# Optimization experiments

Measured on AMD Instinct MI355X. Metric: run time of the kernel, lower is better.

Reference implementation:

```python
import jax, jax.numpy as jnp
import numpy as np

N_NODES = 100000
N_EDGES = 1600000
IN = 128
HID = 128
EPS = 1e-5


def setup_inputs() -> dict:
    key = jax.random.key(0)
    ks = jax.random.split(key, 20)
    def lin(k, fi, fo):
        return jax.random.normal(k, (fi, fo), dtype=jnp.float32) / np.sqrt(fi)
    inp = {
        'x': jax.random.normal(ks[0], (N_NODES, IN), dtype=jnp.float32),
        'src': jax.random.randint(ks[1], (N_EDGES,), 0, N_NODES),
        'dst': jax.random.randint(ks[2], (N_EDGES,), 0, N_NODES),
        # SAGEConv layer 1..3: fc_self, fc_neigh, bias
        'Wself1': lin(ks[3], IN, HID), 'Wneigh1': lin(ks[4], IN, HID), 'b1': jnp.zeros((HID,), jnp.float32),
        'Wself2': lin(ks[5], HID, HID), 'Wneigh2': lin(ks[6], HID, HID), 'b2': jnp.zeros((HID,), jnp.float32),
        'Wself3': lin(ks[7], HID, HID), 'Wneigh3': lin(ks[8], HID, HID), 'b3': jnp.zeros((HID,), jnp.float32),
        # shared BatchNorm1d(hid)
        'gamma': jnp.ones((HID,), jnp.float32), 'beta': jnp.zeros((HID,), jnp.float32),
        # decoder MLP hid->hid->hid->1
        'Wd1': lin(ks[9], HID, HID), 'bd1': jnp.zeros((HID,), jnp.float32),
        'Wd2': lin(ks[10], HID, HID), 'bd2': jnp.zeros((HID,), jnp.float32),
        'Wd3': lin(ks[11], HID, 1), 'bd3': jnp.zeros((1,), jnp.float32),
    }
    return inp


def _sage_conv(h, src, dst, deg, Wself, Wneigh, b, n):
    # mean aggregation over in-neighbors: gather + segment-sum + divide
    neigh_sum = jax.ops.segment_sum(h[src], dst, num_segments=n)  # [N, F]
    neigh_mean = neigh_sum / deg[:, None]
    return h @ Wself + neigh_mean @ Wneigh + b


def _batch_norm(h, gamma, beta):
    mu = jnp.mean(h, axis=0)
    var = jnp.mean(jnp.square(h - mu), axis=0)  # biased var, as torch BN training
    return gamma * (h - mu) * jax.lax.rsqrt(var + EPS) + beta


def reference(x, src, dst, Wself1, Wneigh1, b1, Wself2, Wneigh2, b2,
              Wself3, Wneigh3, b3, gamma, beta, Wd1, bd1, Wd2, bd2, Wd3, bd3):
    n = x.shape[0]
    deg = jax.ops.segment_sum(jnp.ones_like(dst, dtype=x.dtype), dst, num_segments=n)
    deg = jnp.maximum(deg, 1.0)
    h = _sage_conv(x, src, dst, deg, Wself1, Wneigh1, b1, n)
    h = jax.nn.relu(_batch_norm(h, gamma, beta))  # dropout = identity (eval)
    h = _sage_conv(h, src, dst, deg, Wself2, Wneigh2, b2, n)
    h = jax.nn.relu(_batch_norm(h, gamma, beta))
    h = _sage_conv(h, src, dst, deg, Wself3, Wneigh3, b3, n)
    # decoder MLP
    h = jax.nn.relu(h @ Wd1 + bd1)
    h = jax.nn.relu(h @ Wd2 + bd2)
    return h @ Wd3 + bd3  # [N, 1]
```

## Files before the change

kernel.cpp:

```cpp
#include <hip/hip_runtime.h>

typedef unsigned short u16;
typedef unsigned int u32;
using bf16x8 = __attribute__((ext_vector_type(8))) __bf16;
using f32x4  = __attribute__((ext_vector_type(4))) float;

#define CAP 48

__global__ void SAGE_79328045957727_kernel() {}

__device__ __forceinline__ float bf2f(u16 u) {
  union { u32 i; float f; } v; v.i = ((u32)u) << 16; return v.f;
}
__device__ __forceinline__ u16 f2bf(float f) {
  union { float f; u32 i; } v; v.f = f;
  u32 x = v.i;
  return (u16)((x + 0x7FFFu + ((x >> 16) & 1u)) >> 16);
}


__global__ void zero_kernel(int* p, int n) {
  int i = blockIdx.x * 256 + threadIdx.x;
  if (i < n) p[i] = 0;
}


__global__ __launch_bounds__(256) void build_kernel(
    const int* __restrict__ src, const int* __restrict__ dst,
    int* __restrict__ deg, int* __restrict__ csr, int E, int npart,
    const float* __restrict__ x, u16* __restrict__ xb, long nelem4,
    const float* w0, const float* w1, const float* w2, const float* w3,
    const float* w4, const float* w5, const float* w6, const float* w7,
    u16* __restrict__ wt) {
  int b = blockIdx.x;
  if (b < 1024) {
    int p = b & 7;
    int brank = b >> 3;
    int lo = p * npart, hi = lo + npart;
    for (int i = brank * 256 + threadIdx.x; i < E; i += 128 * 256) {
      int dv = dst[i];
      if (dv >= lo && dv < hi) {
        int pos = atomicAdd(&deg[dv], 1);
        if (pos < CAP) csr[(size_t)dv * CAP + pos] = src[i];
      }
    }
  } else if (b < 1280) {
    long t = (long)(b - 1024) * 256 + threadIdx.x;
    for (long i4 = t; i4 < nelem4; i4 += 256 * 256) {
      float4 v = ((const float4*)x)[i4];
      u32* op = (u32*)(xb + i4 * 4);
      op[0] = ((u32)f2bf(v.y) << 16) | (u32)f2bf(v.x);
      op[1] = ((u32)f2bf(v.w) << 16) | (u32)f2bf(v.z);
    }
  } else {
    int tg = (b - 1280) * 256 + threadIdx.x;
    for (int k = 0; k < 8; ++k) {
      int idx = tg + k * 16384;
      int m = idx >> 14;
      int i = idx & 16383;
      const float* W = m == 0 ? w0 : m == 1 ? w1 : m == 2 ? w2 : m == 3 ? w3
                     : m == 4 ? w4 : m == 5 ? w5 : m == 6 ? w6 : w7;
      int r = i >> 7, c = i & 127;
      wt[(size_t)m * 16384 + (size_t)c * 128 + r] = f2bf(W[i]);
    }
  }
}


template <int BNIN>
__global__ __launch_bounds__(256) void gather_mean_kernel(
    const u16* __restrict__ H, const int* __restrict__ csr,
    const int* __restrict__ deg, const float* __restrict__ stats,
    const float* __restrict__ gamma, const float* __restrict__ beta,
    u16* __restrict__ M, int N, float invN) {
  __shared__ float sSc[128], sSh[128];
  if (BNIN) {
    int t = threadIdx.x;
    if (t < 128) {
      float mu = stats[t] * invN;
      float var = stats[128 + t] * invN - mu * mu;
      float is = rsqrtf(var + 1e-5f);
      float sc = gamma[t] * is;
      sSc[t] = sc;
      sSh[t] = beta[t] - mu * sc;
    }
    __syncthreads();
  }
  int node = blockIdx.x * 16 + (threadIdx.x >> 4);
  if (node >= N) return;
  int lane = threadIdx.x & 15;
  int fo = lane * 8;
  float sc[8], sh[8];
  if (BNIN) {
    for (int j = 0; j < 8; ++j) { sc[j] = sSc[fo + j]; sh[j] = sSh[fo + j]; }
  }
  const int* nl = csr + (size_t)node * CAP;
  int d = deg[node];
  int dm = d < CAP ? d : CAP;
  float a0=0.f,a1=0.f,a2=0.f,a3=0.f,a4=0.f,a5=0.f,a6=0.f,a7=0.f;

#define ACCQ(q) do { \
    float e0 = bf2f((u16)((q).x & 0xffffu)), e1 = bf2f((u16)((q).x >> 16)); \
    float e2 = bf2f((u16)((q).y & 0xffffu)), e3 = bf2f((u16)((q).y >> 16)); \
    float e4 = bf2f((u16)((q).z & 0xffffu)), e5 = bf2f((u16)((q).z >> 16)); \
    float e6 = bf2f((u16)((q).w & 0xffffu)), e7 = bf2f((u16)((q).w >> 16)); \
    if (BNIN) { \
      e0 = fmaxf(sc[0]*e0+sh[0], 0.f); e1 = fmaxf(sc[1]*e1+sh[1], 0.f); \
      e2 = fmaxf(sc[2]*e2+sh[2], 0.f); e3 = fmaxf(sc[3]*e3+sh[3], 0.f); \
      e4 = fmaxf(sc[4]*e4+sh[4], 0.f); e5 = fmaxf(sc[5]*e5+sh[5], 0.f); \
      e6 = fmaxf(sc[6]*e6+sh[6], 0.f); e7 = fmaxf(sc[7]*e7+sh[7], 0.f); \
    } \
    a0 += e0; a1 += e1; a2 += e2; a3 += e3; \
    a4 += e4; a5 += e5; a6 += e6; a7 += e7; \
  } while (0)

  int e = 0;
  for (; e + 4 <= dm; e += 4) {
    int i0 = nl[e], i1 = nl[e + 1], i2 = nl[e + 2], i3 = nl[e + 3];
    uint4 q0 = *(const uint4*)(H + (size_t)i0 * 128 + fo);
    uint4 q1 = *(const uint4*)(H + (size_t)i1 * 128 + fo);
    uint4 q2 = *(const uint4*)(H + (size_t)i2 * 128 + fo);
    uint4 q3 = *(const uint4*)(H + (size_t)i3 * 128 + fo);
    ACCQ(q0); ACCQ(q1); ACCQ(q2); ACCQ(q3);
  }
  for (; e < dm; ++e) {
    uint4 q = *(const uint4*)(H + (size_t)nl[e] * 128 + fo);
    ACCQ(q);
  }
#undef ACCQ
  float inv = 1.f / (float)(d > 0 ? d : 1);
  uint4 o;
  o.x = ((u32)f2bf(a1 * inv) << 16) | (u32)f2bf(a0 * inv);
  o.y = ((u32)f2bf(a3 * inv) << 16) | (u32)f2bf(a2 * inv);
  o.z = ((u32)f2bf(a5 * inv) << 16) | (u32)f2bf(a4 * inv);
  o.w = ((u32)f2bf(a7 * inv) << 16) | (u32)f2bf(a6 * inv);
  *(uint4*)(M + (size_t)node * 128 + fo) = o;
}


#define LDSROW 136

template <int BNIN>
__global__ __launch_bounds__(256) void gemm_mfma(
    const u16* __restrict__ A, const u16* __restrict__ B,
    const u16* __restrict__ W1t, const u16* __restrict__ W2t,
    const float* __restrict__ bias, u16* __restrict__ C,
    float* __restrict__ statsOut, const float* __restrict__ statsIn,
    const float* __restrict__ gamma, const float* __restrict__ beta,
    int N, float invN) {
  __shared__ u16 sT[128 * LDSROW];
  __shared__ float sSc[128], sSh[128];

  int tid = threadIdx.x;
  int wave = tid >> 6;
  int lane = tid & 63;
  int l15 = lane & 15;
  int quad = lane >> 4;
  size_t row0 = (size_t)blockIdx.x * 128;

  if (BNIN) {
    if (tid < 128) {
      float mu = statsIn[tid] * invN;
      float var = statsIn[128 + tid] * invN - mu * mu;
      float is = rsqrtf(var + 1e-5f);
      float sc = gamma[tid] * is;
      sSc[tid] = sc;
      sSh[tid] = beta[tid] - mu * sc;
    }
    __syncthreads();
  }

  float bsc[8], bsh[8];
  int cbase = ((tid * 4) & 63) * 2;
  if (BNIN) {
    for (int j = 0; j < 8; ++j) { bsc[j] = sSc[cbase + j]; bsh[j] = sSh[cbase + j]; }
  }

  f32x4 acc[8][2];
  for (int rt = 0; rt < 8; ++rt)
    for (int ct = 0; ct < 2; ++ct)
      for (int i = 0; i < 4; ++i) acc[rt][ct][i] = 0.f;

  bf16x8 wf[2][4];

  for (int ph = 0; ph < 2; ++ph) {
    const u16* Asrc = ph ? B : A;
    const u16* Wt = ph ? W2t : W1t;

    for (int ct = 0; ct < 2; ++ct) {
      int col = wave * 32 + ct * 16 + l15;
      for (int kk = 0; kk < 4; ++kk)
        wf[ct][kk] = *(const bf16x8*)(Wt + (size_t)col * 128 + kk * 32 + quad * 8);
    }

    if (ph) __syncthreads();
    for (int j = 0; j < 8; ++j) {
      int idx = j * 1024 + tid * 4;
      int r = idx >> 6;
      int c = idx & 63;
      size_t grow = row0 + r;
      if (grow >= (size_t)N) grow = (size_t)(N - 1);
      const u32* gp = (const u32*)(Asrc + grow * 128) + c;
      u32 v0 = gp[0], v1 = gp[1], v2 = gp[2], v3 = gp[3];
      if (BNIN && ph == 0) {
        float e0 = fmaxf(bsc[0]*bf2f((u16)(v0 & 0xffffu))+bsh[0], 0.f);
        float e1 = fmaxf(bsc[1]*bf2f((u16)(v0 >> 16))+bsh[1], 0.f);
        float e2 = fmaxf(bsc[2]*bf2f((u16)(v1 & 0xffffu))+bsh[2], 0.f);
        float e3 = fmaxf(bsc[3]*bf2f((u16)(v1 >> 16))+bsh[3], 0.f);
        float e4 = fmaxf(bsc[4]*bf2f((u16)(v2 & 0xffffu))+bsh[4], 0.f);
        float e5 = fmaxf(bsc[5]*bf2f((u16)(v2 >> 16))+bsh[5], 0.f);
        float e6 = fmaxf(bsc[6]*bf2f((u16)(v3 & 0xffffu))+bsh[6], 0.f);
        float e7 = fmaxf(bsc[7]*bf2f((u16)(v3 >> 16))+bsh[7], 0.f);
        v0 = ((u32)f2bf(e1) << 16) | (u32)f2bf(e0);
        v1 = ((u32)f2bf(e3) << 16) | (u32)f2bf(e2);
        v2 = ((u32)f2bf(e5) << 16) | (u32)f2bf(e4);
        v3 = ((u32)f2bf(e7) << 16) | (u32)f2bf(e6);
      }
      u32* lp = (u32*)(sT + (size_t)r * LDSROW + c * 2);
      lp[0] = v0; lp[1] = v1; lp[2] = v2; lp[3] = v3;
    }
    __syncthreads();

    for (int kk = 0; kk < 4; ++kk) {
      int kbase = kk * 32 + quad * 8;
      for (int rt = 0; rt < 8; ++rt) {
        bf16x8 af = *(const bf16x8*)(sT + (size_t)(rt * 16 + l15) * LDSROW + kbase);
        acc[rt][0] = __builtin_amdgcn_mfma_f32_16x16x32_bf16(af, wf[0][kk], acc[rt][0], 0, 0, 0);
        acc[rt][1] = __builtin_amdgcn_mfma_f32_16x16x32_bf16(af, wf[1][kk], acc[rt][1], 0, 0, 0);
      }
    }
  }

  for (int ct = 0; ct < 2; ++ct) {
    int col = wave * 32 + ct * 16 + l15;
    float bv = bias[col];
    float ssum = 0.f, ssq = 0.f;
    for (int rt = 0; rt < 8; ++rt) {
      for (int i = 0; i < 4; ++i) {
        size_t row = row0 + rt * 16 + quad * 4 + i;
        if (row < (size_t)N) {
          float v = acc[rt][ct][i] + bv;
          C[row * 128 + col] = f2bf(v);
          ssum += v; ssq += v * v;
        }
      }
    }
    for (int o = 16; o < 64; o <<= 1) {
      ssum += __shfl_xor(ssum, o);
      ssq  += __shfl_xor(ssq, o);
    }
    if (quad == 0) {
      atomicAdd(&statsOut[col], ssum);
      atomicAdd(&statsOut[128 + col], ssq);
    }
  }
}


__global__ __launch_bounds__(256) void megagemm(
    const u16* __restrict__ ZB, const u16* __restrict__ M,
    const u16* __restrict__ wtS3, const u16* __restrict__ wtN3,
    const float* __restrict__ b3,
    const u16* __restrict__ wtD1, const float* __restrict__ bd1,
    const u16* __restrict__ wtD2, const float* __restrict__ bd2,
    const float* __restrict__ wd3, const float* __restrict__ bd3,
    const float* __restrict__ statsIn, const float* __restrict__ gamma,
    const float* __restrict__ beta,
    float* __restrict__ outF, int N, float invN) {
  __shared__ u16 sT[128 * LDSROW];
  __shared__ float sSc[128], sSh[128];
  __shared__ float sOut[128];

  int tid = threadIdx.x;
  int wave = tid >> 6;
  int lane = tid & 63;
  int l15 = lane & 15;
  int quad = lane >> 4;
  size_t row0 = (size_t)blockIdx.x * 128;

  if (tid < 128) {
    float mu = statsIn[tid] * invN;
    float var = statsIn[128 + tid] * invN - mu * mu;
    float is = rsqrtf(var + 1e-5f);
    float sc = gamma[tid] * is;
    sSc[tid] = sc;
    sSh[tid] = beta[tid] - mu * sc;
    sOut[tid] = 0.f;
  }
  __syncthreads();

  float bsc[8], bsh[8];
  int cbase = ((tid * 4) & 63) * 2;
  for (int j = 0; j < 8; ++j) { bsc[j] = sSc[cbase + j]; bsh[j] = sSh[cbase + j]; }

  f32x4 acc[8][2];
  for (int rt = 0; rt < 8; ++rt)
    for (int ct = 0; ct < 2; ++ct)
      for (int i = 0; i < 4; ++i) acc[rt][ct][i] = 0.f;

  bf16x8 wf[2][4];

  for (int ph = 0; ph < 2; ++ph) {
    const u16* Asrc = ph ? M : ZB;
    const u16* Wt = ph ? wtN3 : wtS3;

    for (int ct = 0; ct < 2; ++ct) {
      int col = wave * 32 + ct * 16 + l15;
      for (int kk = 0; kk < 4; ++kk)
        wf[ct][kk] = *(const bf16x8*)(Wt + (size_t)col * 128 + kk * 32 + quad * 8);
    }

    if (ph) __syncthreads();
    for (int j = 0; j < 8; ++j) {
      int idx = j * 1024 + tid * 4;
      int r = idx >> 6;
      int c = idx & 63;
      size_t grow = row0 + r;
      if (grow >= (size_t)N) grow = (size_t)(N - 1);
      const u32* gp = (const u32*)(Asrc + grow * 128) + c;
      u32 v0 = gp[0], v1 = gp[1], v2 = gp[2], v3 = gp[3];
      if (ph == 0) {
        float e0 = fmaxf(bsc[0]*bf2f((u16)(v0 & 0xffffu))+bsh[0], 0.f);
        float e1 = fmaxf(bsc[1]*bf2f((u16)(v0 >> 16))+bsh[1], 0.f);
        float e2 = fmaxf(bsc[2]*bf2f((u16)(v1 & 0xffffu))+bsh[2], 0.f);
        float e3 = fmaxf(bsc[3]*bf2f((u16)(v1 >> 16))+bsh[3], 0.f);
        float e4 = fmaxf(bsc[4]*bf2f((u16)(v2 & 0xffffu))+bsh[4], 0.f);
        float e5 = fmaxf(bsc[5]*bf2f((u16)(v2 >> 16))+bsh[5], 0.f);
        float e6 = fmaxf(bsc[6]*bf2f((u16)(v3 & 0xffffu))+bsh[6], 0.f);
        float e7 = fmaxf(bsc[7]*bf2f((u16)(v3 >> 16))+bsh[7], 0.f);
        v0 = ((u32)f2bf(e1) << 16) | (u32)f2bf(e0);
        v1 = ((u32)f2bf(e3) << 16) | (u32)f2bf(e2);
        v2 = ((u32)f2bf(e5) << 16) | (u32)f2bf(e4);
        v3 = ((u32)f2bf(e7) << 16) | (u32)f2bf(e6);
      }
      u32* lp = (u32*)(sT + (size_t)r * LDSROW + c * 2);
      lp[0] = v0; lp[1] = v1; lp[2] = v2; lp[3] = v3;
    }
    __syncthreads();

    for (int kk = 0; kk < 4; ++kk) {
      int kbase = kk * 32 + quad * 8;
      for (int rt = 0; rt < 8; ++rt) {
        bf16x8 af = *(const bf16x8*)(sT + (size_t)(rt * 16 + l15) * LDSROW + kbase);
        acc[rt][0] = __builtin_amdgcn_mfma_f32_16x16x32_bf16(af, wf[0][kk], acc[rt][0], 0, 0, 0);
        acc[rt][1] = __builtin_amdgcn_mfma_f32_16x16x32_bf16(af, wf[1][kk], acc[rt][1], 0, 0, 0);
      }
    }
  }

  for (int g = 0; g < 2; ++g) {
    const u16* Wt = g ? wtD2 : wtD1;
    const float* bs = g ? bd1 : b3;
    int do_relu = g;

    __syncthreads();
    for (int ct = 0; ct < 2; ++ct) {
      int col = wave * 32 + ct * 16 + l15;
      float bv = bs[col];
      for (int rt = 0; rt < 8; ++rt) {
        for (int i = 0; i < 4; ++i) {
          int row = rt * 16 + quad * 4 + i;
          float v = acc[rt][ct][i] + bv;
          if (do_relu) v = fmaxf(v, 0.f);
          sT[(size_t)row * LDSROW + col] = f2bf(v);
        }
      }
    }
    __syncthreads();

    for (int ct = 0; ct < 2; ++ct) {
      int col = wave * 32 + ct * 16 + l15;
      for (int kk = 0; kk < 4; ++kk)
        wf[ct][kk] = *(const bf16x8*)(Wt + (size_t)col * 128 + kk * 32 + quad * 8);
    }
    for (int rt = 0; rt < 8; ++rt)
      for (int ct = 0; ct < 2; ++ct)
        for (int i = 0; i < 4; ++i) acc[rt][ct][i] = 0.f;
    for (int kk = 0; kk < 4; ++kk) {
      int kbase = kk * 32 + quad * 8;
      for (int rt = 0; rt < 8; ++rt) {
        bf16x8 af = *(const bf16x8*)(sT + (size_t)(rt * 16 + l15) * LDSROW + kbase);
        acc[rt][0] = __builtin_amdgcn_mfma_f32_16x16x32_bf16(af, wf[0][kk], acc[rt][0], 0, 0, 0);
        acc[rt][1] = __builtin_amdgcn_mfma_f32_16x16x32_bf16(af, wf[1][kk], acc[rt][1], 0, 0, 0);
      }
    }
  }

  {
    int col0 = wave * 32 + l15;
    float bv0 = bd2[col0], bv1 = bd2[col0 + 16];
    float w30 = wd3[col0], w31 = wd3[col0 + 16];
    for (int rt = 0; rt < 8; ++rt) {
      for (int i = 0; i < 4; ++i) {
        size_t row = row0 + rt * 16 + quad * 4 + i;
        float v0 = fmaxf(acc[rt][0][i] + bv0, 0.f);
        float v1 = fmaxf(acc[rt][1][i] + bv1, 0.f);
        float pv = v0 * w30 + v1 * w31;
        pv += __shfl_xor(pv, 1);
        pv += __shfl_xor(pv, 2);
        pv += __shfl_xor(pv, 4);
        pv += __shfl_xor(pv, 8);
        if (l15 == 0 && row < (size_t)N)
          atomicAdd(&sOut[rt * 16 + quad * 4 + i], pv);
      }
    }
    __syncthreads();
    if (tid < 128) {
      size_t row = row0 + tid;
      if (row < (size_t)N) outF[row] = sOut[tid] + bd3[0];
    }
  }
}


extern "C" void kernel_launch(void* const* d_in, const int* in_sizes, int n_in,
                              void* d_out, int out_size, void* d_ws, size_t ws_size,
                              hipStream_t stream) {
  const float* x      = (const float*)d_in[0];
  const int*   src    = (const int*)d_in[1];
  const int*   dst    = (const int*)d_in[2];
  const float* Wself1 = (const float*)d_in[3];
  const float* Wneigh1= (const float*)d_in[4];
  const float* b1     = (const float*)d_in[5];
  const float* Wself2 = (const float*)d_in[6];
  const float* Wneigh2= (const float*)d_in[7];
  const float* b2     = (const float*)d_in[8];
  const float* Wself3 = (const float*)d_in[9];
  const float* Wneigh3= (const float*)d_in[10];
  const float* b3     = (const float*)d_in[11];
  const float* gamma  = (const float*)d_in[12];
  const float* beta   = (const float*)d_in[13];
  const float* Wd1    = (const float*)d_in[14];
  const float* bd1    = (const float*)d_in[15];
  const float* Wd2    = (const float*)d_in[16];
  const float* bd2    = (const float*)d_in[17];
  const float* Wd3    = (const float*)d_in[18];
  const float* bd3    = (const float*)d_in[19];
  float* out = (float*)d_out;

  int N = in_sizes[0] / 128;
  int E = in_sizes[1];
  int npart = (N + 7) / 8;

  char* ws = (char*)d_ws;
  size_t off = 0;
  int* deg; int* csr; float* stats1; float* stats2;
  u16* xb; u16* ZA; u16* ZB; u16* M; u16* wt;
  deg   = (int*)(ws + off);   off += (size_t)N * 4;
  stats1= (float*)(ws + off); off += 256 * 4;
  stats2= (float*)(ws + off); off += 256 * 4;
  off = (off + 511) & ~(size_t)511;
  csr  = (int*)(ws + off);   off += ((size_t)N * CAP * 4 + 511) & ~(size_t)511;
  wt   = (u16*)(ws + off);   off += ((size_t)8 * 16384 * 2 + 511) & ~(size_t)511;
  xb   = (u16*)(ws + off);   off += ((size_t)N * 128 * 2 + 511) & ~(size_t)511;
  ZA   = (u16*)(ws + off);   off += ((size_t)N * 128 * 2 + 511) & ~(size_t)511;
  ZB   = (u16*)(ws + off);   off += ((size_t)N * 128 * 2 + 511) & ~(size_t)511;
  M    = (u16*)(ws + off);   off += ((size_t)N * 128 * 2 + 511) & ~(size_t)511;

  u16* wtS1 = wt + 0 * 16384; u16* wtN1 = wt + 1 * 16384;
  u16* wtS2 = wt + 2 * 16384; u16* wtN2 = wt + 3 * 16384;
  u16* wtS3 = wt + 4 * 16384; u16* wtN3 = wt + 5 * 16384;
  u16* wtD1 = wt + 6 * 16384; u16* wtD2 = wt + 7 * 16384;

  zero_kernel<<<(N + 512 + 255) / 256, 256, 0, stream>>>(deg, N + 512);

  long nelem4 = (long)N * 128 / 4;
  build_kernel<<<1344, 256, 0, stream>>>(
      src, dst, deg, csr, E, npart, x, xb, nelem4,
      Wself1, Wneigh1, Wself2, Wneigh2, Wself3, Wneigh3, Wd1, Wd2, wt);

  int strips = (N + 127) / 128;
  int g16    = (N + 15) / 16;
  float invN = 1.f / (float)N;

  gather_mean_kernel<0><<<g16, 256, 0, stream>>>(
      xb, csr, deg, (const float*)0, (const float*)0, (const float*)0, M, N, invN);
  gemm_mfma<0><<<strips, 256, 0, stream>>>(
      xb, M, wtS1, wtN1, b1, ZA, stats1, (const float*)0, (const float*)0,
      (const float*)0, N, invN);

  gather_mean_kernel<1><<<g16, 256, 0, stream>>>(
      ZA, csr, deg, stats1, gamma, beta, M, N, invN);
  gemm_mfma<1><<<strips, 256, 0, stream>>>(
      ZA, M, wtS2, wtN2, b2, ZB, stats2, stats1, gamma, beta, N, invN);

  gather_mean_kernel<1><<<g16, 256, 0, stream>>>(
      ZB, csr, deg, stats2, gamma, beta, M, N, invN);
  megagemm<<<strips, 256, 0, stream>>>(
      ZB, M, wtS3, wtN3, b3, wtD1, bd1, wtD2, bd2, Wd3, bd3,
      stats2, gamma, beta, out, N, invN);
}
```

Before: 540.6 us.

## Fuse neighbor gather-mean into GEMM tiles and precompute BN+ReLU activations once

The neighbor mean aggregation now runs inside the GEMM kernels, written straight into the shared-memory tile, so the aggregated matrix M no longer makes a round trip through global memory. BatchNorm+ReLU is applied once per layer by a separate elementwise kernel, instead of being recomputed on every gathered neighbor row and again in the GEMM staging. This trades three gather kernels for two cheap elementwise passes. The risk is that the gather inside a 128-row GEMM block, at 256 threads per block, may expose less memory-level parallelism than the standalone gather kernel did.

Measured after the change: 649.6 us. 1.2x slower.

```diff
diff --git a/kernel.cpp b/kernel.cpp
--- a/kernel.cpp
+++ b/kernel.cpp
@@ -6,6 +6,7 @@
 using f32x4  = __attribute__((ext_vector_type(4))) float;
 
 #define CAP 48
+#define LDSROW 136
 
 __global__ void SAGE_79328045957727_kernel() {}
 
@@ -67,90 +68,126 @@
 }
 
 
-template <int BNIN>
-__global__ __launch_bounds__(256) void gather_mean_kernel(
-    const u16* __restrict__ H, const int* __restrict__ csr,
-    const int* __restrict__ deg, const float* __restrict__ stats,
-    const float* __restrict__ gamma, const float* __restrict__ beta,
-    u16* __restrict__ M, int N, float invN) {
+__global__ __launch_bounds__(256) void bnrelu_kernel(
+    const u16* __restrict__ Z, u16* __restrict__ G,
+    const float* __restrict__ stats, const float* __restrict__ gamma,
+    const float* __restrict__ beta, long n4, float invN) {
   __shared__ float sSc[128], sSh[128];
-  if (BNIN) {
-    int t = threadIdx.x;
-    if (t < 128) {
-      float mu = stats[t] * invN;
-      float var = stats[128 + t] * invN - mu * mu;
-      float is = rsqrtf(var + 1e-5f);
-      float sc = gamma[t] * is;
-      sSc[t] = sc;
-      sSh[t] = beta[t] - mu * sc;
-    }
-    __syncthreads();
-  }
-  int node = blockIdx.x * 16 + (threadIdx.x >> 4);
-  if (node >= N) return;
-  int lane = threadIdx.x & 15;
-  int fo = lane * 8;
-  float sc[8], sh[8];
-  if (BNIN) {
-    for (int j = 0; j < 8; ++j) { sc[j] = sSc[fo + j]; sh[j] = sSh[fo + j]; }
-  }
-  const int* nl = csr + (size_t)node * CAP;
-  int d = deg[node];
-  int dm = d < CAP ? d : CAP;
-  float a0=0.f,a1=0.f,a2=0.f,a3=0.f,a4=0.f,a5=0.f,a6=0.f,a7=0.f;
-
-#define ACCQ(q) do { \
-    float e0 = bf2f((u16)((q).x & 0xffffu)), e1 = bf2f((u16)((q).x >> 16)); \
-    float e2 = bf2f((u16)((q).y & 0xffffu)), e3 = bf2f((u16)((q).y >> 16)); \
-    float e4 = bf2f((u16)((q).z & 0xffffu)), e5 = bf2f((u16)((q).z >> 16)); \
-    float e6 = bf2f((u16)((q).w & 0xffffu)), e7 = bf2f((u16)((q).w >> 16)); \
-    if (BNIN) { \
-      e0 = fmaxf(sc[0]*e0+sh[0], 0.f); e1 = fmaxf(sc[1]*e1+sh[1], 0.f); \
-      e2 = fmaxf(sc[2]*e2+sh[2], 0.f); e3 = fmaxf(sc[3]*e3+sh[3], 0.f); \
-      e4 = fmaxf(sc[4]*e4+sh[4], 0.f); e5 = fmaxf(sc[5]*e5+sh[5], 0.f); \
-      e6 = fmaxf(sc[6]*e6+sh[6], 0.f); e7 = fmaxf(sc[7]*e7+sh[7], 0.f); \
-    } \
-    a0 += e0; a1 += e1; a2 += e2; a3 += e3; \
-    a4 += e4; a5 += e5; a6 += e6; a7 += e7; \
+  int t = threadIdx.x;
+  if (t < 128) {
+    float mu = stats[t] * invN;
+    float var = stats[128 + t] * invN - mu * mu;
+    float is = rsqrtf(var + 1e-5f);
+    float sc = gamma[t] * is;
+    sSc[t] = sc;
+    sSh[t] = beta[t] - mu * sc;
+  }
+  __syncthreads();
+  for (long i4 = (long)blockIdx.x * 256 + t; i4 < n4; i4 += (long)gridDim.x * 256) {
+    uint4 q = ((const uint4*)Z)[i4];
+    int c0 = ((int)(i4 & 15)) * 8;
+    float e0 = fmaxf(sSc[c0+0]*bf2f((u16)(q.x & 0xffffu))+sSh[c0+0], 0.f);
+    float e1 = fmaxf(sSc[c0+1]*bf2f((u16)(q.x >> 16))    +sSh[c0+1], 0.f);
+    float e2 = fmaxf(sSc[c0+2]*bf2f((u16)(q.y & 0xffffu))+sSh[c0+2], 0.f);
+    float e3 = fmaxf(sSc[c0+3]*bf2f((u16)(q.y >> 16))    +sSh[c0+3], 0.f);
+    float e4 = fmaxf(sSc[c0+4]*bf2f((u16)(q.z & 0xffffu))+sSh[c0+4], 0.f);
+    float e5 = fmaxf(sSc[c0+5]*bf2f((u16)(q.z >> 16))    +sSh[c0+5], 0.f);
+    float e6 = fmaxf(sSc[c0+6]*bf2f((u16)(q.w & 0xffffu))+sSh[c0+6], 0.f);
+    float e7 = fmaxf(sSc[c0+7]*bf2f((u16)(q.w >> 16))    +sSh[c0+7], 0.f);
+    uint4 o;
+    o.x = ((u32)f2bf(e1) << 16) | (u32)f2bf(e0);
+    o.y = ((u32)f2bf(e3) << 16) | (u32)f2bf(e2);
+    o.z = ((u32)f2bf(e5) << 16) | (u32)f2bf(e4);
+    o.w = ((u32)f2bf(e7) << 16) | (u32)f2bf(e6);
+    ((uint4*)G)[i4] = o;
+  }
+}
+
+
+__device__ __forceinline__ void gather_tile(
+    const u16* __restrict__ G, const int* __restrict__ csr,
+    const int* __restrict__ deg, u16* sT, size_t row0, int N, int tid) {
+  int lf = tid & 15;
+  int slot = tid >> 4;
+  int fo = lf * 8;
+#define ACC8(q) do { \
+    a0 += bf2f((u16)((q).x & 0xffffu)); a1 += bf2f((u16)((q).x >> 16)); \
+    a2 += bf2f((u16)((q).y & 0xffffu)); a3 += bf2f((u16)((q).y >> 16)); \
+    a4 += bf2f((u16)((q).z & 0xffffu)); a5 += bf2f((u16)((q).z >> 16)); \
+    a6 += bf2f((u16)((q).w & 0xffffu)); a7 += bf2f((u16)((q).w >> 16)); \
   } while (0)
-
-  int e = 0;
-  for (; e + 4 <= dm; e += 4) {
-    int i0 = nl[e], i1 = nl[e + 1], i2 = nl[e + 2], i3 = nl[e + 3];
-    uint4 q0 = *(const uint4*)(H + (size_t)i0 * 128 + fo);
-    uint4 q1 = *(const uint4*)(H + (size_t)i1 * 128 + fo);
-    uint4 q2 = *(const uint4*)(H + (size_t)i2 * 128 + fo);
-    uint4 q3 = *(const uint4*)(H + (size_t)i3 * 128 + fo);
-    ACCQ(q0); ACCQ(q1); ACCQ(q2); ACCQ(q3);
-  }
-  for (; e < dm; ++e) {
-    uint4 q = *(const uint4*)(H + (size_t)nl[e] * 128 + fo);
-    ACCQ(q);
-  }
-#undef ACCQ
-  float inv = 1.f / (float)(d > 0 ? d : 1);
-  uint4 o;
-  o.x = ((u32)f2bf(a1 * inv) << 16) | (u32)f2bf(a0 * inv);
-  o.y = ((u32)f2bf(a3 * inv) << 16) | (u32)f2bf(a2 * inv);
-  o.z = ((u32)f2bf(a5 * inv) << 16) | (u32)f2bf(a4 * inv);
-  o.w = ((u32)f2bf(a7 * inv) << 16) | (u32)f2bf(a6 * inv);
-  *(uint4*)(M + (size_t)node * 128 + fo) = o;
-}
-
-
-#define LDSROW 136
-
-template <int BNIN>
-__global__ __launch_bounds__(256) void gemm_mfma(
-    const u16* __restrict__ A, const u16* __restrict__ B,
-    const u16* __restrict__ W1t, const u16* __restrict__ W2t,
-    const float* __restrict__ bias, u16* __restrict__ C,
-    float* __restrict__ statsOut, const float* __restrict__ statsIn,
-    const float* __restrict__ gamma, const float* __restrict__ beta,
-    int N, float invN) {
+  for (int it = 0; it < 8; ++it) {
+    int r = it * 16 + slot;
+    size_t node = row0 + r;
+    int d = (node < (size_t)N) ? deg[node] : 0;
+    int dm = d < CAP ? d : CAP;
+    const int* nl = csr + (node < (size_t)N ? node : 0) * CAP;
+    float a0=0.f,a1=0.f,a2=0.f,a3=0.f,a4=0.f,a5=0.f,a6=0.f,a7=0.f;
+    int e = 0;
+    for (; e + 4 <= dm; e += 4) {
+      int i0 = nl[e], i1 = nl[e + 1], i2 = nl[e + 2], i3 = nl[e + 3];
+      uint4 q0 = *(const uint4*)(G + (size_t)i0 * 128 + fo);
+      uint4 q1 = *(const uint4*)(G + (size_t)i1 * 128 + fo);
+      uint4 q2 = *(const uint4*)(G + (size_t)i2 * 128 + fo);
+      uint4 q3 = *(const uint4*)(G + (size_t)i3 * 128 + fo);
+      ACC8(q0); ACC8(q1); ACC8(q2); ACC8(q3);
+    }
+    for (; e < dm; ++e) {
+      uint4 q = *(const uint4*)(G + (size_t)nl[e] * 128 + fo);
+      ACC8(q);
+    }
+    float inv = 1.f / (float)(d > 0 ? d : 1);
+    u32 o0 = ((u32)f2bf(a1 * inv) << 16) | (u32)f2bf(a0 * inv);
+    u32 o1 = ((u32)f2bf(a3 * inv) << 16) | (u32)f2bf(a2 * inv);
+    u32 o2 = ((u32)f2bf(a5 * inv) << 16) | (u32)f2bf(a4 * inv);
+    u32 o3 = ((u32)f2bf(a7 * inv) << 16) | (u32)f2bf(a6 * inv);
+    u32* lp = (u32*)(sT + (size_t)r * LDSROW) + lf * 4;
+    lp[0] = o0; lp[1] = o1; lp[2] = o2; lp[3] = o3;
+  }
+#undef ACC8
+}
+
+__device__ __forceinline__ void stage_tile(
+    const u16* __restrict__ A, u16* sT, size_t row0, int N, int tid) {
+  for (int j = 0; j < 8; ++j) {
+    int idx = j * 1024 + tid * 4;
+    int r = idx >> 6;
+    int c = idx & 63;
+    size_t grow = row0 + r;
+    if (grow >= (size_t)N) grow = (size_t)(N - 1);
+    const u32* gp = (const u32*)(A + grow * 128) + c;
+    u32 v0 = gp[0], v1 = gp[1], v2 = gp[2], v3 = gp[3];
+    u32* lp = (u32*)(sT + (size_t)r * LDSROW + c * 2);
+    lp[0] = v0; lp[1] = v1; lp[2] = v2; lp[3] = v3;
+  }
+}
+
+__device__ __forceinline__ void mfma_tile(
+    const u16* sT, const u16* __restrict__ Wt, f32x4 acc[8][2],
+    int wave, int l15, int quad) {
+  bf16x8 wf[2][4];
+  for (int ct = 0; ct < 2; ++ct) {
+    int col = wave * 32 + ct * 16 + l15;
+    for (int kk = 0; kk < 4; ++kk)
+      wf[ct][kk] = *(const bf16x8*)(Wt + (size_t)col * 128 + kk * 32 + quad * 8);
+  }
+  for (int kk = 0; kk < 4; ++kk) {
+    int kbase = kk * 32 + quad * 8;
+    for (int rt = 0; rt < 8; ++rt) {
+      bf16x8 af = *(const bf16x8*)(sT + (size_t)(rt * 16 + l15) * LDSROW + kbase);
+      acc[rt][0] = __builtin_amdgcn_mfma_f32_16x16x32_bf16(af, wf[0][kk], acc[rt][0], 0, 0, 0);
+      acc[rt][1] = __builtin_amdgcn_mfma_f32_16x16x32_bf16(af, wf[1][kk], acc[rt][1], 0, 0, 0);
+    }
+  }
+}
+
+
+__global__ __launch_bounds__(256) void gemm_fused(
+    const u16* __restrict__ G, const int* __restrict__ csr,
+    const int* __restrict__ deg, const u16* __restrict__ Wst,
+    const u16* __restrict__ Wnt, const float* __restrict__ bias,
+    u16* __restrict__ C, float* __restrict__ statsOut, int N) {
   __shared__ u16 sT[128 * LDSROW];
-  __shared__ float sSc[128], sSh[128];
-
   int tid = threadIdx.x;
   int wave = tid >> 6;
   int lane = tid & 63;
@@ -158,78 +195,19 @@
   int quad = lane >> 4;
   size_t row0 = (size_t)blockIdx.x * 128;
 
-  if (BNIN) {
-    if (tid < 128) {
-      float mu = statsIn[tid] * invN;
-      float var = statsIn[128 + tid] * invN - mu * mu;
-      float is = rsqrtf(var + 1e-5f);
-      float sc = gamma[tid] * is;
-      sSc[tid] = sc;
-      sSh[tid] = beta[tid] - mu * sc;
-    }
-    __syncthreads();
-  }
-
-  float bsc[8], bsh[8];
-  int cbase = ((tid * 4) & 63) * 2;
-  if (BNIN) {
-    for (int j = 0; j < 8; ++j) { bsc[j] = sSc[cbase + j]; bsh[j] = sSh[cbase + j]; }
-  }
-
   f32x4 acc[8][2];
   for (int rt = 0; rt < 8; ++rt)
     for (int ct = 0; ct < 2; ++ct)
       for (int i = 0; i < 4; ++i) acc[rt][ct][i] = 0.f;
 
-  bf16x8 wf[2][4];
-
-  for (int ph = 0; ph < 2; ++ph) {
-    const u16* Asrc = ph ? B : A;
-    const u16* Wt = ph ? W2t : W1t;
-
-    for (int ct = 0; ct < 2; ++ct) {
-      int col = wave * 32 + ct * 16 + l15;
-      for (int kk = 0; kk < 4; ++kk)
-        wf[ct][kk] = *(const bf16x8*)(Wt + (size_t)col * 128 + kk * 32 + quad * 8);
-    }
-
-    if (ph) __syncthreads();
-    for (int j = 0; j < 8; ++j) {
-      int idx = j * 1024 + tid * 4;
-      int r = idx >> 6;
-      int c = idx & 63;
-      size_t grow = row0 + r;
-      if (grow >= (size_t)N) grow = (size_t)(N - 1);
-      const u32* gp = (const u32*)(Asrc + grow * 128) + c;
-      u32 v0 = gp[0], v1 = gp[1], v2 = gp[2], v3 = gp[3];
-      if (BNIN && ph == 0) {
-        float e0 = fmaxf(bsc[0]*bf2f((u16)(v0 & 0xffffu))+bsh[0], 0.f);
-        float e1 = fmaxf(bsc[1]*bf2f((u16)(v0 >> 16))+bsh[1], 0.f);
-        float e2 = fmaxf(bsc[2]*bf2f((u16)(v1 & 0xffffu))+bsh[2], 0.f);
-        float e3 = fmaxf(bsc[3]*bf2f((u16)(v1 >> 16))+bsh[3], 0.f);
-        float e4 = fmaxf(bsc[4]*bf2f((u16)(v2 & 0xffffu))+bsh[4], 0.f);
-        float e5 = fmaxf(bsc[5]*bf2f((u16)(v2 >> 16))+bsh[5], 0.f);
-        float e6 = fmaxf(bsc[6]*bf2f((u16)(v3 & 0xffffu))+bsh[6], 0.f);
-        float e7 = fmaxf(bsc[7]*bf2f((u16)(v3 >> 16))+bsh[7], 0.f);
-        v0 = ((u32)f2bf(e1) << 16) | (u32)f2bf(e0);
-        v1 = ((u32)f2bf(e3) << 16) | (u32)f2bf(e2);
-        v2 = ((u32)f2bf(e5) << 16) | (u32)f2bf(e4);
-        v3 = ((u32)f2bf(e7) << 16) | (u32)f2bf(e6);
-      }
-      u32* lp = (u32*)(sT + (size_t)r * LDSROW + c * 2);
-      lp[0] = v0; lp[1] = v1; lp[2] = v2; lp[3] = v3;
-    }
-    __syncthreads();
-
-    for (int kk = 0; kk < 4; ++kk) {
-      int kbase = kk * 32 + quad * 8;
-      for (int rt = 0; rt < 8; ++rt) {
-        bf16x8 af = *(const bf16x8*)(sT + (size_t)(rt * 16 + l15) * LDSROW + kbase);
-        acc[rt][0] = __builtin_amdgcn_mfma_f32_16x16x32_bf16(af, wf[0][kk], acc[rt][0], 0, 0, 0);
-        acc[rt][1] = __builtin_amdgcn_mfma_f32_16x16x32_bf16(af, wf[1][kk], acc[rt][1], 0, 0, 0);
-      }
-    }
-  }
+  gather_tile(G, csr, deg, sT, row0, N, tid);
+  __syncthreads();
+  mfma_tile(sT, Wnt, acc, wave, l15, quad);
+  __syncthreads();
+
+  stage_tile(G, sT, row0, N, tid);
+  __syncthreads();
+  mfma_tile(sT, Wst, acc, wave, l15, quad);
 
   for (int ct = 0; ct < 2; ++ct) {
     int col = wave * 32 + ct * 16 + l15;
@@ -258,17 +236,15 @@
 
 
 __global__ __launch_bounds__(256) void megagemm(
-    const u16* __restrict__ ZB, const u16* __restrict__ M,
+    const u16* __restrict__ G, const int* __restrict__ csr,
+    const int* __restrict__ deg,
     const u16* __restrict__ wtS3, const u16* __restrict__ wtN3,
     const float* __restrict__ b3,
     const u16* __restrict__ wtD1, const float* __restrict__ bd1,
     const u16* __restrict__ wtD2, const float* __restrict__ bd2,
     const float* __restrict__ wd3, const float* __restrict__ bd3,
-    const float* __restrict__ statsIn, const float* __restrict__ gamma,
-    const float* __restrict__ beta,
-    float* __restrict__ outF, int N, float invN) {
+    float* __restrict__ outF, int N) {
   __shared__ u16 sT[128 * LDSROW];
-  __shared__ float sSc[128], sSh[128];
   __shared__ float sOut[128];
 
   int tid = threadIdx.x;
@@ -278,75 +254,20 @@
   int quad = lane >> 4;
   size_t row0 = (size_t)blockIdx.x * 128;
 
-  if (tid < 128) {
-    float mu = statsIn[tid] * invN;
-    float var = statsIn[128 + tid] * invN - mu * mu;
-    float is = rsqrtf(var + 1e-5f);
-    float sc = gamma[tid] * is;
-    sSc[tid] = sc;
-    sSh[tid] = beta[tid] - mu * sc;
-    sOut[tid] = 0.f;
-  }
-  __syncthreads();
-
-  float bsc[8], bsh[8];
-  int cbase = ((tid * 4) & 63) * 2;
-  for (int j = 0; j < 8; ++j) { bsc[j] = sSc[cbase + j]; bsh[j] = sSh[cbase + j]; }
+  if (tid < 128) sOut[tid] = 0.f;
 
   f32x4 acc[8][2];
   for (int rt = 0; rt < 8; ++rt)
     for (int ct = 0; ct < 2; ++ct)
       for (int i = 0; i < 4; ++i) acc[rt][ct][i] = 0.f;
 
-  bf16x8 wf[2][4];
-
-  for (int ph = 0; ph < 2; ++ph) {
-    const u16* Asrc = ph ? M : ZB;
-    const u16* Wt = ph ? wtN3 : wtS3;
-
-    for (int ct = 0; ct < 2; ++ct) {
-      int col = wave * 32 + ct * 16 + l15;
-      for (int kk = 0; kk < 4; ++kk)
-        wf[ct][kk] = *(const bf16x8*)(Wt + (size_t)col * 128 + kk * 32 + quad * 8);
-    }
-
-    if (ph) __syncthreads();
-    for (int j = 0; j < 8; ++j) {
-      int idx = j * 1024 + tid * 4;
-      int r = idx >> 6;
-      int c = idx & 63;
-      size_t grow = row0 + r;
-      if (grow >= (size_t)N) grow = (size_t)(N - 1);
-      const u32* gp = (const u32*)(Asrc + grow * 128) + c;
-      u32 v0 = gp[0], v1 = gp[1], v2 = gp[2], v3 = gp[3];
-      if (ph == 0) {
-        float e0 = fmaxf(bsc[0]*bf2f((u16)(v0 & 0xffffu))+bsh[0], 0.f);
-        float e1 = fmaxf(bsc[1]*bf2f((u16)(v0 >> 16))+bsh[1], 0.f);
-        float e2 = fmaxf(bsc[2]*bf2f((u16)(v1 & 0xffffu))+bsh[2], 0.f);
-        float e3 = fmaxf(bsc[3]*bf2f((u16)(v1 >> 16))+bsh[3], 0.f);
-        float e4 = fmaxf(bsc[4]*bf2f((u16)(v2 & 0xffffu))+bsh[4], 0.f);
-        float e5 = fmaxf(bsc[5]*bf2f((u16)(v2 >> 16))+bsh[5], 0.f);
-        float e6 = fmaxf(bsc[6]*bf2f((u16)(v3 & 0xffffu))+bsh[6], 0.f);
-        float e7 = fmaxf(bsc[7]*bf2f((u16)(v3 >> 16))+bsh[7], 0.f);
-        v0 = ((u32)f2bf(e1) << 16) | (u32)f2bf(e0);
-        v1 = ((u32)f2bf(e3) << 16) | (u32)f2bf(e2);
-        v2 = ((u32)f2bf(e5) << 16) | (u32)f2bf(e4);
-        v3 = ((u32)f2bf(e7) << 16) | (u32)f2bf(e6);
-      }
-      u32* lp = (u32*)(sT + (size_t)r * LDSROW + c * 2);
-      lp[0] = v0; lp[1] = v1; lp[2] = v2; lp[3] = v3;
-    }
-    __syncthreads();
-
-    for (int kk = 0; kk < 4; ++kk) {
-      int kbase = kk * 32 + quad * 8;
-      for (int rt = 0; rt < 8; ++rt) {
-        bf16x8 af = *(const bf16x8*)(sT + (size_t)(rt * 16 + l15) * LDSROW + kbase);
-        acc[rt][0] = __builtin_amdgcn_mfma_f32_16x16x32_bf16(af, wf[0][kk], acc[rt][0], 0, 0, 0);
-        acc[rt][1] = __builtin_amdgcn_mfma_f32_16x16x32_bf16(af, wf[1][kk], acc[rt][1], 0, 0, 0);
-      }
-    }
-  }
+  gather_tile(G, csr, deg, sT, row0, N, tid);
+  __syncthreads();
+  mfma_tile(sT, wtN3, acc, wave, l15, quad);
+  __syncthreads();
+  stage_tile(G, sT, row0, N, tid);
+  __syncthreads();
+  mfma_tile(sT, wtS3, acc, wave, l15, quad);
 
   for (int g = 0; g < 2; ++g) {
     const u16* Wt = g ? wtD2 : wtD1;
@@ -368,22 +289,10 @@
     }
     __syncthreads();
 
-    for (int ct = 0; ct < 2; ++ct) {
-      int col = wave * 32 + ct * 16 + l15;
-      for (int kk = 0; kk < 4; ++kk)
-        wf[ct][kk] = *(const bf16x8*)(Wt + (size_t)col * 128 + kk * 32 + quad * 8);
-    }
     for (int rt = 0; rt < 8; ++rt)
       for (int ct = 0; ct < 2; ++ct)
         for (int i = 0; i < 4; ++i) acc[rt][ct][i] = 0.f;
-    for (int kk = 0; kk < 4; ++kk) {
-      int kbase = kk * 32 + quad * 8;
-      for (int rt = 0; rt < 8; ++rt) {
-        bf16x8 af = *(const bf16x8*)(sT + (size_t)(rt * 16 + l15) * LDSROW + kbase);
-        acc[rt][0] = __builtin_amdgcn_mfma_f32_16x16x32_bf16(af, wf[0][kk], acc[rt][0], 0, 0, 0);
-        acc[rt][1] = __builtin_amdgcn_mfma_f32_16x16x32_bf16(af, wf[1][kk], acc[rt][1], 0, 0, 0);
-      }
-    }
+    mfma_tile(sT, Wt, acc, wave, l15, quad);
   }
 
   {
@@ -462,6 +371,9 @@
   u16* wtS3 = wt + 4 * 16384; u16* wtN3 = wt + 5 * 16384;
   u16* wtD1 = wt + 6 * 16384; u16* wtD2 = wt + 7 * 16384;
 
+  u16* GA = M;
+  u16* GB = ZA;
+
   zero_kernel<<<(N + 512 + 255) / 256, 256, 0, stream>>>(deg, N + 512);
 
   long nelem4 = (long)N * 128 / 4;
@@ -470,23 +382,19 @@
       Wself1, Wneigh1, Wself2, Wneigh2, Wself3, Wneigh3, Wd1, Wd2, wt);
 
   int strips = (N + 127) / 128;
-  int g16    = (N + 15) / 16;
   float invN = 1.f / (float)N;
-
-  gather_mean_kernel<0><<<g16, 256, 0, stream>>>(
-      xb, csr, deg, (const float*)0, (const float*)0, (const float*)0, M, N, invN);
-  gemm_mfma<0><<<strips, 256, 0, stream>>>(
-      xb, M, wtS1, wtN1, b1, ZA, stats1, (const float*)0, (const float*)0,
-      (const float*)0, N, invN);
-
-  gather_mean_kernel<1><<<g16, 256, 0, stream>>>(
-      ZA, csr, deg, stats1, gamma, beta, M, N, invN);
-  gemm_mfma<1><<<strips, 256, 0, stream>>>(
-      ZA, M, wtS2, wtN2, b2, ZB, stats2, stats1, gamma, beta, N, invN);
-
-  gather_mean_kernel<1><<<g16, 256, 0, stream>>>(
-      ZB, csr, deg, stats2, gamma, beta, M, N, invN);
+  long n4 = (long)N * 16;
+
+  gemm_fused<<<strips, 256, 0, stream>>>(
+      xb, csr, deg, wtS1, wtN1, b1, ZA, stats1, N);
+
+  bnrelu_kernel<<<2048, 256, 0, stream>>>(ZA, GA, stats1, gamma, beta, n4, invN);
+
+  gemm_fused<<<strips, 256, 0, stream>>>(
+      GA, csr, deg, wtS2, wtN2, b2, ZB, stats2, N);
+
+  bnrelu_kernel<<<2048, 256, 0, stream>>>(ZB, GB, stats2, gamma, beta, n4, invN);
+
   megagemm<<<strips, 256, 0, stream>>>(
-      ZB, M, wtS3, wtN3, b3, wtD1, bd1, wtD2, bd2, Wd3, bd3,
-      stats2, gamma, beta, out, N, invN);
-}
+      GB, csr, deg, wtS3, wtN3, b3, wtD1, bd1, wtD2, bd2, Wd3, bd3, out, N);
+}
```
